# Performance work log

Hardware: AMD Instinct MI355X
Metric: run time of the kernel (lower is better)

Reference implementation:

```python
import jax, jax.numpy as jnp
import numpy as np
import math

N = 100000
E = 800000
H = 256
TDIM = 32
NTYPES = 22
NLAYERS = 2


def layer_norm(x, g, b, eps=1e-5):
    mu = jnp.mean(x, axis=-1, keepdims=True)
    var = jnp.var(x, axis=-1, keepdims=True)
    return (x - mu) * jax.lax.rsqrt(var + eps) * g + b


def setup_inputs() -> dict:
    key = jax.random.key(0)
    ks = jax.random.split(key, 16)
    s = 1.0 / math.sqrt(H)
    inp = {
        "clause_reprs": jax.random.normal(ks[0], (N, H), dtype=jnp.float32),
        "timestamps": jax.random.uniform(ks[1], (N,), dtype=jnp.float32) * 10000.0,
        "deriv_types": jax.random.randint(ks[2], (N,), 0, NTYPES),
        "derivation_edges": jax.random.randint(ks[3], (2, E), 0, N),
        # params
        "emb_table": jax.random.normal(ks[4], (NTYPES, H), dtype=jnp.float32),
        "temp_W": jax.random.normal(ks[5], (TDIM, H), dtype=jnp.float32) / math.sqrt(TDIM),
        "temp_b": jnp.zeros((H,), jnp.float32),
        "fus_W1": jax.random.normal(ks[6], (3 * H, H), dtype=jnp.float32) / math.sqrt(3 * H),
        "fus_b1": jnp.zeros((H,), jnp.float32),
        "fus_W2": jax.random.normal(ks[7], (H, H), dtype=jnp.float32) * s,
        "fus_b2": jnp.zeros((H,), jnp.float32),
        "in_g": jnp.ones((H,), jnp.float32),
        "in_b": jnp.zeros((H,), jnp.float32),
        "deriv_W": jax.random.normal(ks[8], (NLAYERS, 2 * H, H), dtype=jnp.float32) / math.sqrt(2 * H),
        "deriv_b": jnp.zeros((NLAYERS, H), jnp.float32),
        "dn_g": jnp.ones((NLAYERS, H), jnp.float32),
        "dn_b": jnp.zeros((NLAYERS, H), jnp.float32),
    }
    return inp


def reference(clause_reprs, timestamps, deriv_types, derivation_edges,
              emb_table, temp_W, temp_b, fus_W1, fus_b1, fus_W2, fus_b2,
              in_g, in_b, deriv_W, deriv_b, dn_g, dn_b):
    # --- temporal sinusoidal encoding -> projection ---
    half = TDIM // 2
    freqs = jnp.exp(-math.log(10000.0) * jnp.arange(half, dtype=jnp.float32) / half)
    angles = timestamps[:, None] * freqs[None, :]                      # (N, half)
    pe = jnp.concatenate([jnp.sin(angles), jnp.cos(angles)], axis=-1)  # (N, TDIM)
    temporal_enc = pe @ temp_W + temp_b                                # (N, H)
    # --- derivation type embedding ---
    deriv_enc = emb_table[deriv_types]                                 # (N, H)
    # --- input fusion + residual + LN ---
    cat = jnp.concatenate([clause_reprs, temporal_enc, deriv_enc], axis=-1)
    fused = jax.nn.relu(cat @ fus_W1 + fus_b1) @ fus_W2 + fus_b2
    x = layer_norm(fused + clause_reprs, in_g, in_b)
    # --- derivation message passing along DAG edges (parent -> child) ---
    src, dst = derivation_edges[0], derivation_edges[1]
    count = jnp.zeros((N, 1), jnp.float32).at[dst].add(1.0)
    count = jnp.maximum(count, 1.0)
    for l in range(NLAYERS):
        parent_msgs = x[src]                                           # (E, H) gather
        agg = jnp.zeros_like(x).at[dst].add(parent_msgs) / count       # (N, H) scatter-add
        combined = jnp.concatenate([x, agg], axis=-1)                  # (N, 2H)
        update = jax.nn.relu(combined @ deriv_W[l] + deriv_b[l])
        x = layer_norm(x + update, dn_g[l], dn_b[l])
    return x
```

## Files before the change

### kernel.cpp

```cpp
#include <hip/hip_runtime.h>
#include <hip/hip_bf16.h>
#include <math.h>

#define N_NODES 100000
#define N_EDGES 800000
#define H 256
#define NTYPES 22
#define SCAN_G 98
#define GRID5 ((N_NODES + 127) / 128)

typedef __attribute__((ext_vector_type(8))) short short8;
typedef __attribute__((ext_vector_type(4))) float f32x4;
typedef unsigned short u16;

__device__ __forceinline__ u16 f2bf(float f) {
    unsigned u = __float_as_uint(f);
    u += 0x7FFF + ((u >> 16) & 1);
    return (u16)(u >> 16);
}
__device__ __forceinline__ float bf2f(u16 u) {
    return __uint_as_float(((unsigned)u) << 16);
}
__device__ __forceinline__ int pi2(int k) {
    return (k & 192) | ((k & 3) << 4) | ((k >> 2) & 15);
}

__device__ __forceinline__ void gload16(const void* g, void* l) {
    __builtin_amdgcn_global_load_lds(
        (const __attribute__((address_space(1))) unsigned int*)g,
        (__attribute__((address_space(3))) unsigned int*)l, 16, 0, 0);
}

__global__ __launch_bounds__(256) void conv_bf16(
    const float* __restrict__ src, u16* __restrict__ dst)
{
    size_t i = (size_t)blockIdx.x * 256 + threadIdx.x;
    const float4 a = ((const float4*)src)[i * 2];
    const float4 b = ((const float4*)src)[i * 2 + 1];
    short8 v;
    v[0] = (short)f2bf(a.x); v[1] = (short)f2bf(a.y);
    v[2] = (short)f2bf(a.z); v[3] = (short)f2bf(a.w);
    v[4] = (short)f2bf(b.x); v[5] = (short)f2bf(b.y);
    v[6] = (short)f2bf(b.z); v[7] = (short)f2bf(b.w);
    ((short8*)dst)[i] = v;
}

__global__ __launch_bounds__(256) void prep_small(
    const float* __restrict__ temp_W, const float* __restrict__ temp_b,
    const float* __restrict__ emb, const float* __restrict__ fus_W1,
    const float* __restrict__ fus_b1,
    float* __restrict__ C1, float* __restrict__ C2, float* __restrict__ beff)
{
    int b = blockIdx.x;
    int j = threadIdx.x;
    if (b < 32) {
        float acc = 0.f;
        #pragma unroll 8
        for (int m = 0; m < H; ++m)
            acc += temp_W[b * H + m] * fus_W1[(size_t)(H + m) * H + j];
        C1[b * H + j] = acc;
    } else if (b < 32 + NTYPES) {
        int e = b - 32;
        float acc = 0.f;
        #pragma unroll 8
        for (int m = 0; m < H; ++m)
            acc += emb[e * H + m] * fus_W1[(size_t)(2 * H + m) * H + j];
        C2[e * H + j] = acc;
    } else {
        float acc = fus_b1[j];
        #pragma unroll 8
        for (int m = 0; m < H; ++m)
            acc += temp_b[m] * fus_W1[(size_t)(H + m) * H + j];
        beff[j] = acc;
    }
}

__global__ __launch_bounds__(256) void prep_frag(
    const float* __restrict__ fus_W1, const float* __restrict__ C1,
    const float* __restrict__ fus_W2, const float* __restrict__ deriv_W,
    u16* __restrict__ wblob)
{
    int s = blockIdx.x;
    #pragma unroll
    for (int it = 0; it < 4; ++it) {
        int c = it * 256 + threadIdx.x;
        int l = c & 63, nt = c >> 6;
        int ncol = (nt << 4) | (l & 15);
        int kin = (l >> 4) << 3;
        short8 v;
        #pragma unroll
        for (int i = 0; i < 8; ++i) {
            const float* srcp;
            if (s < 8) {
                srcp = fus_W1 + (size_t)(s * 32 + kin + i) * H;
            } else if (s == 8) {
                srcp = C1 + (size_t)(kin + i) * H;
            } else if (s < 17) {
                int k = (s - 9) * 32 + kin + i;
                srcp = fus_W2 + (size_t)pi2(k) * H;
            } else if (s < 33) {
                int k = (s - 17) * 32 + kin + i;
                srcp = deriv_W + (size_t)((k >> 8) * 256 + pi2(k & 255)) * H;
            } else {
                int k = (s - 33) * 32 + kin + i;
                srcp = deriv_W + (size_t)(512 + (k >> 8) * 256 + pi2(k & 255)) * H;
            }
            v[i] = (short)f2bf(srcp[ncol]);
        }
        *reinterpret_cast<short8*>(wblob + (size_t)s * 8192 + (size_t)c * 8) = v;
    }
}

__global__ void count_kernel(const int* __restrict__ dst, int* __restrict__ cnt)
{
    int e = blockIdx.x * blockDim.x + threadIdx.x;
    if (e < N_EDGES) atomicAdd(&cnt[dst[e]], 1);
}

__global__ __launch_bounds__(1024) void scan1_kernel(
    const int* __restrict__ cnt, int* __restrict__ off, int* __restrict__ bsum)
{
    __shared__ int s[1024];
    int i = blockIdx.x * 1024 + threadIdx.x;
    int v = (i < N_NODES) ? cnt[i] : 0;
    s[threadIdx.x] = v;
    __syncthreads();
    #pragma unroll
    for (int o = 1; o < 1024; o <<= 1) {
        int t = (threadIdx.x >= o) ? s[threadIdx.x - o] : 0;
        __syncthreads();
        s[threadIdx.x] += t;
        __syncthreads();
    }
    if (i < N_NODES) off[i] = s[threadIdx.x];
    if (threadIdx.x == 1023) bsum[blockIdx.x] = s[1023];
}

__global__ void scan2_kernel(const int* __restrict__ bsum, int* __restrict__ bbase)
{
    if (threadIdx.x == 0) {
        int acc = 0;
        for (int b = 0; b < SCAN_G; ++b) { bbase[b] = acc; acc += bsum[b]; }
    }
}

__global__ __launch_bounds__(1024) void scan3_kernel(
    int* __restrict__ off, const int* __restrict__ bbase,
    const int* __restrict__ cnt, int* __restrict__ cursor)
{
    int i = blockIdx.x * 1024 + threadIdx.x;
    if (i < N_NODES) {
        int incl = off[i] + bbase[blockIdx.x];
        off[i] = incl;
        cursor[i] = incl - cnt[i];
    }
}

__global__ void fill_kernel(const int* __restrict__ src, const int* __restrict__ dst,
                            int* __restrict__ cursor, int* __restrict__ csr)
{
    int e = blockIdx.x * blockDim.x + threadIdx.x;
    if (e < N_EDGES) {
        int pos = atomicAdd(&cursor[dst[e]], 1);
        csr[pos] = src[e];
    }
}

__global__ __launch_bounds__(256) void gather_kernel(
    const u16* __restrict__ xb, const int* __restrict__ csr,
    const int* __restrict__ off, const int* __restrict__ cnt,
    u16* __restrict__ agg)
{
    int node = blockIdx.x * 4 + (threadIdx.x >> 6);
    int l = threadIdx.x & 63;
    int half = l >> 5, lc = l & 31;
    int deg = cnt[node];
    int start = off[node] - deg;
    float a[8] = {0.f, 0.f, 0.f, 0.f, 0.f, 0.f, 0.f, 0.f};
    int j = half;
    for (; j + 2 < deg; j += 4) {
        int s0 = csr[start + j];
        int s1 = csr[start + j + 2];
        short8 v0 = *reinterpret_cast<const short8*>(xb + (size_t)s0 * H + lc * 8);
        short8 v1 = *reinterpret_cast<const short8*>(xb + (size_t)s1 * H + lc * 8);
        #pragma unroll
        for (int i = 0; i < 8; ++i)
            a[i] += bf2f((u16)v0[i]) + bf2f((u16)v1[i]);
    }
    if (j < deg) {
        int s0 = csr[start + j];
        short8 v0 = *reinterpret_cast<const short8*>(xb + (size_t)s0 * H + lc * 8);
        #pragma unroll
        for (int i = 0; i < 8; ++i)
            a[i] += bf2f((u16)v0[i]);
    }
    #pragma unroll
    for (int i = 0; i < 8; ++i)
        a[i] += __shfl_xor(a[i], 32);
    if (half == 0) {
        float sc = 1.0f / fmaxf((float)deg, 1.0f);
        short8 o;
        #pragma unroll
        for (int i = 0; i < 8; ++i) o[i] = (short)f2bf(a[i] * sc);
        *reinterpret_cast<short8*>(agg + (size_t)node * H + lc * 8) = o;
    }
}

__device__ __forceinline__ void mfma_regs(const short8 a[4], const short8 b[4],
                                          f32x4 acc[4][4])
{
    #pragma unroll
    for (int n = 0; n < 4; ++n)
        #pragma unroll
        for (int m = 0; m < 4; ++m)
            acc[m][n] = __builtin_amdgcn_mfma_f32_16x16x32_bf16(a[m], b[n],
                                                                acc[m][n], 0, 0, 0);
}

__global__ __launch_bounds__(512, 4) void k1_mfma(
    const u16* __restrict__ cb, const float* __restrict__ ts,
    const int* __restrict__ types, const u16* __restrict__ wblob,
    const float* __restrict__ C2, const float* __restrict__ beff,
    u16* __restrict__ hb)
{
    __shared__ __align__(16) u16 Asm[32768];
    __shared__ __align__(16) u16 pes[4096];
    int tid = threadIdx.x, w = tid >> 6, l = tid & 63;
    int wm = w >> 2, wn = w & 3, g = l >> 4, c0 = l & 15;
    int i0 = blockIdx.x * 128;

    #pragma unroll
    for (int j = 0; j < 8; ++j) {
        int rt = j * 16 + (tid >> 5);
        int grow = min(i0 + rt, N_NODES - 1);
        int gl = (l & 31) ^ (rt & 7);
        gload16(cb + (size_t)grow * H + gl * 8,
                Asm + (size_t)rt * 256 + (l & 31) * 8);
    }
    {
        int prow = tid >> 2, kq = tid & 3;
        float tsv = ts[min(i0 + prow, N_NODES - 1)];
        short8 v;
        #pragma unroll
        for (int i = 0; i < 8; ++i) {
            int k = kq * 8 + i;
            float fr = expf(-0.57564627324851f * (float)(k & 15));
            float ang = tsv * fr;
            v[i] = (short)f2bf((k < 16) ? sinf(ang) : cosf(ang));
        }
        *reinterpret_cast<short8*>(pes + prow * 32 + ((kq ^ (prow & 3)) << 3)) = v;
    }
    __syncthreads();

    f32x4 acc[4][4] = {};
    #pragma unroll
    for (int t = 0; t < 9; ++t) {
        short8 a[4], b[4];
        #pragma unroll
        for (int m = 0; m < 4; ++m) {
            int row = (((wm << 2) | m) << 4) + c0;
            if (t < 8) {
                int c = t * 4 + g;
                a[m] = *reinterpret_cast<const short8*>(
                    Asm + row * 256 + ((c ^ (c0 & 7)) << 3));
            } else {
                a[m] = *reinterpret_cast<const short8*>(
                    pes + row * 32 + ((g ^ (c0 & 3)) << 3));
            }
        }
        #pragma unroll
        for (int n = 0; n < 4; ++n)
            b[n] = *reinterpret_cast<const short8*>(
                wblob + (size_t)t * 8192 + (size_t)(((((wn << 2) | n) << 6) | l) << 3));
        mfma_regs(a, b, acc);
    }

    float bev[4];
    #pragma unroll
    for (int n = 0; n < 4; ++n) bev[n] = beff[(((wn << 2) | n) << 4) | c0];
    #pragma unroll
    for (int m = 0; m < 4; ++m) {
        #pragma unroll
        for (int r = 0; r < 4; ++r) {
            int rl = (((wm << 2) | m) << 4) + (g << 2) + r;
            int row = i0 + rl;
            bool ok = row < N_NODES;
            int tp = types[ok ? row : 0];
            const float* c2r = C2 + (size_t)tp * H;
            ushort4 o;
            float v0 = fmaxf(acc[m][0][r] + bev[0] + c2r[((wn << 2) << 4) | c0], 0.f);
            float v1 = fmaxf(acc[m][1][r] + bev[1] + c2r[(((wn << 2) | 1) << 4) | c0], 0.f);
            float v2 = fmaxf(acc[m][2][r] + bev[2] + c2r[(((wn << 2) | 2) << 4) | c0], 0.f);
            float v3 = fmaxf(acc[m][3][r] + bev[3] + c2r[(((wn << 2) | 3) << 4) | c0], 0.f);
            o.x = f2bf(v0); o.y = f2bf(v1); o.z = f2bf(v2); o.w = f2bf(v3);
            if (ok)
                *reinterpret_cast<ushort4*>(hb + (size_t)row * H + (wn << 6) + (c0 << 2)) = o;
        }
    }
}

__global__ __launch_bounds__(512, 4) void k2_mfma(
    const u16* __restrict__ hb, const u16* __restrict__ cb,
    const u16* __restrict__ wblob, const float* __restrict__ b2,
    const float* __restrict__ gW, const float* __restrict__ bW,
    u16* __restrict__ xb)
{
    __shared__ __align__(16) u16 Asm[32768];
    __shared__ float2 red[512];
    int tid = threadIdx.x, w = tid >> 6, l = tid & 63;
    int wm = w >> 2, wn = w & 3, g = l >> 4, c0 = l & 15;
    int i0 = blockIdx.x * 128;

    #pragma unroll
    for (int j = 0; j < 8; ++j) {
        int rt = j * 16 + (tid >> 5);
        int grow = min(i0 + rt, N_NODES - 1);
        int gl = (l & 31) ^ (rt & 7);
        gload16(hb + (size_t)grow * H + gl * 8,
                Asm + (size_t)rt * 256 + (l & 31) * 8);
    }
    __syncthreads();

    f32x4 acc[4][4] = {};
    #pragma unroll
    for (int t = 0; t < 8; ++t) {
        short8 a[4], b[4];
        #pragma unroll
        for (int m = 0; m < 4; ++m) {
            int row = (((wm << 2) | m) << 4) + c0;
            int c = t * 4 + g;
            a[m] = *reinterpret_cast<const short8*>(
                Asm + row * 256 + ((c ^ (c0 & 7)) << 3));
        }
        #pragma unroll
        for (int n = 0; n < 4; ++n)
            b[n] = *reinterpret_cast<const short8*>(
                wblob + (size_t)t * 8192 + (size_t)(((((wn << 2) | n) << 6) | l) << 3));
        mfma_regs(a, b, acc);
    }

    float bv[4], gv[4], bbv[4];
    int lc[4];
    #pragma unroll
    for (int n = 0; n < 4; ++n) {
        lc[n] = (((wn << 2) | n) << 4) | c0;
        bv[n] = b2[lc[n]]; gv[n] = gW[lc[n]]; bbv[n] = bW[lc[n]];
    }
    #pragma unroll
    for (int m = 0; m < 4; ++m) {
        #pragma unroll
        for (int r = 0; r < 4; ++r) {
            int rl = (((wm << 2) | m) << 4) + (g << 2) + r;
            int rowc = min(i0 + rl, N_NODES - 1);
            const u16* cr = cb + (size_t)rowc * H;
            float s = 0.f, q = 0.f;
            #pragma unroll
            for (int n = 0; n < 4; ++n) {
                float pv = acc[m][n][r] + bv[n] + bf2f(cr[lc[n]]);
                acc[m][n][r] = pv;
                s += pv; q += pv * pv;
            }
            #pragma unroll
            for (int o = 1; o < 16; o <<= 1) {
                s += __shfl_xor(s, o);
                q += __shfl_xor(q, o);
            }
            if (c0 == 0) red[(rl << 2) | wn] = make_float2(s, q);
        }
    }
    __syncthreads();
    #pragma unroll
    for (int m = 0; m < 4; ++m) {
        #pragma unroll
        for (int r = 0; r < 4; ++r) {
            int rl = (((wm << 2) | m) << 4) + (g << 2) + r;
            int row = i0 + rl;
            float2 t0 = red[(rl << 2) | 0], t1 = red[(rl << 2) | 1];
            float2 t2 = red[(rl << 2) | 2], t3 = red[(rl << 2) | 3];
            float S = t0.x + t1.x + t2.x + t3.x;
            float Q = t0.y + t1.y + t2.y + t3.y;
            float mu = S * (1.0f / 256.0f);
            float rstd = rsqrtf(Q * (1.0f / 256.0f) - mu * mu + 1e-5f);
            if (row < N_NODES) {
                ushort4 o;
                o.x = f2bf((acc[m][0][r] - mu) * rstd * gv[0] + bbv[0]);
                o.y = f2bf((acc[m][1][r] - mu) * rstd * gv[1] + bbv[1]);
                o.z = f2bf((acc[m][2][r] - mu) * rstd * gv[2] + bbv[2]);
                o.w = f2bf((acc[m][3][r] - mu) * rstd * gv[3] + bbv[3]);
                *reinterpret_cast<ushort4*>(xb + (size_t)row * H + (wn << 6) + (c0 << 2)) = o;
            }
        }
    }
}

template<bool FINAL>
__global__ __launch_bounds__(512, 2) void k5_mfma(
    const u16* __restrict__ xb, const u16* __restrict__ aggb,
    const u16* __restrict__ wblob, const float* __restrict__ bl,
    const float* __restrict__ gl_, const float* __restrict__ bnl,
    u16* __restrict__ xbout, float* __restrict__ xout)
{
    __shared__ __align__(16) u16 Asm[65536];
    __shared__ float2 red[512];
    int tid = threadIdx.x, w = tid >> 6, l = tid & 63;
    int wm = w >> 2, wn = w & 3, g = l >> 4, c0 = l & 15;
    int i0 = blockIdx.x * 128;

    #pragma unroll
    for (int j = 0; j < 16; ++j) {
        int rt = j * 8 + w;
        int grow = min(i0 + rt, N_NODES - 1);
        int gl = l ^ w;
        const u16* src = (gl < 32)
            ? xb + (size_t)grow * H + gl * 8
            : aggb + (size_t)grow * H + (gl - 32) * 8;
        gload16(src, Asm + (size_t)rt * 512 + l * 8);
    }
    __syncthreads();

    f32x4 acc[4][4] = {};
    #pragma unroll
    for (int t = 0; t < 16; ++t) {
        short8 a[4], b[4];
        #pragma unroll
        for (int m = 0; m < 4; ++m) {
            int row = (((wm << 2) | m) << 4) + c0;
            int c = t * 4 + g;
            a[m] = *reinterpret_cast<const short8*>(
                Asm + row * 512 + ((c ^ (c0 & 7)) << 3));
        }
        #pragma unroll
        for (int n = 0; n < 4; ++n)
            b[n] = *reinterpret_cast<const short8*>(
                wblob + (size_t)t * 8192 + (size_t)(((((wn << 2) | n) << 6) | l) << 3));
        mfma_regs(a, b, acc);
    }

    float bv[4], gv[4], bbv[4];
    int lc[4];
    #pragma unroll
    for (int n = 0; n < 4; ++n) {
        lc[n] = (((wn << 2) | n) << 4) | c0;
        bv[n] = bl[lc[n]]; gv[n] = gl_[lc[n]]; bbv[n] = bnl[lc[n]];
    }
    int g0 = (wn << 3) + (c0 >> 1);
    #pragma unroll
    for (int m = 0; m < 4; ++m) {
        #pragma unroll
        for (int r = 0; r < 4; ++r) {
            int rl = (((wm << 2) | m) << 4) + (g << 2) + r;
            ushort4 xr = *reinterpret_cast<const ushort4*>(
                Asm + rl * 512 + ((g0 ^ (rl & 7)) << 3) + ((c0 & 1) << 2));
            float p0 = bf2f(xr.x) + fmaxf(acc[m][0][r] + bv[0], 0.f);
            float p1 = bf2f(xr.y) + fmaxf(acc[m][1][r] + bv[1], 0.f);
            float p2 = bf2f(xr.z) + fmaxf(acc[m][2][r] + bv[2], 0.f);
            float p3 = bf2f(xr.w) + fmaxf(acc[m][3][r] + bv[3], 0.f);
            acc[m][0][r] = p0; acc[m][1][r] = p1;
            acc[m][2][r] = p2; acc[m][3][r] = p3;
            float s = p0 + p1 + p2 + p3;
            float q = p0 * p0 + p1 * p1 + p2 * p2 + p3 * p3;
            #pragma unroll
            for (int o = 1; o < 16; o <<= 1) {
                s += __shfl_xor(s, o);
                q += __shfl_xor(q, o);
            }
            if (c0 == 0) red[(rl << 2) | wn] = make_float2(s, q);
        }
    }
    __syncthreads();
    #pragma unroll
    for (int m = 0; m < 4; ++m) {
        #pragma unroll
        for (int r = 0; r < 4; ++r) {
            int rl = (((wm << 2) | m) << 4) + (g << 2) + r;
            int row = i0 + rl;
            float2 t0 = red[(rl << 2) | 0], t1 = red[(rl << 2) | 1];
            float2 t2 = red[(rl << 2) | 2], t3 = red[(rl << 2) | 3];
            float S = t0.x + t1.x + t2.x + t3.x;
            float Q = t0.y + t1.y + t2.y + t3.y;
            float mu = S * (1.0f / 256.0f);
            float rstd = rsqrtf(Q * (1.0f / 256.0f) - mu * mu + 1e-5f);
            if (row < N_NODES) {
                if (FINAL) {
                    #pragma unroll
                    for (int n = 0; n < 4; ++n)
                        xout[(size_t)row * H + lc[n]] =
                            (acc[m][n][r] - mu) * rstd * gv[n] + bbv[n];
                } else {
                    ushort4 o;
                    o.x = f2bf((acc[m][0][r] - mu) * rstd * gv[0] + bbv[0]);
                    o.y = f2bf((acc[m][1][r] - mu) * rstd * gv[1] + bbv[1]);
                    o.z = f2bf((acc[m][2][r] - mu) * rstd * gv[2] + bbv[2]);
                    o.w = f2bf((acc[m][3][r] - mu) * rstd * gv[3] + bbv[3]);
                    *reinterpret_cast<ushort4*>(
                        xbout + (size_t)row * H + (wn << 6) + (c0 << 2)) = o;
                }
            }
        }
    }
}

extern "C" void kernel_launch(void* const* d_in, const int* in_sizes, int n_in,
                              void* d_out, int out_size, void* d_ws, size_t ws_size,
                              hipStream_t stream)
{
    const float* clause  = (const float*)d_in[0];
    const float* ts      = (const float*)d_in[1];
    const int*   types   = (const int*)  d_in[2];
    const int*   edges   = (const int*)  d_in[3];
    const float* emb     = (const float*)d_in[4];
    const float* temp_W  = (const float*)d_in[5];
    const float* temp_b  = (const float*)d_in[6];
    const float* fus_W1  = (const float*)d_in[7];
    const float* fus_b1  = (const float*)d_in[8];
    const float* fus_W2  = (const float*)d_in[9];
    const float* fus_b2  = (const float*)d_in[10];
    const float* in_g    = (const float*)d_in[11];
    const float* in_b    = (const float*)d_in[12];
    const float* deriv_W = (const float*)d_in[13];
    const float* deriv_b = (const float*)d_in[14];
    const float* dn_g    = (const float*)d_in[15];
    const float* dn_b    = (const float*)d_in[16];

    char* p = (char*)d_ws;
    float* C1   = (float*)p;            p += 32 * H * 4;
    float* C2   = (float*)p;            p += NTYPES * H * 4;
    float* beff = (float*)p;            p += H * 4;
    int* cnt    = (int*)p;              p += N_NODES * 4;
    int* off    = (int*)p;              p += N_NODES * 4;
    int* cursor = (int*)p;              p += N_NODES * 4;
    int* bsum   = (int*)p;              p += 128 * 4;
    int* bbase  = (int*)p;              p += 128 * 4;
    int* csr    = (int*)p;              p += N_EDGES * 4;
    u16* wblob  = (u16*)p;              p += 49 * 8192 * 2;
    u16* B1     = (u16*)p;              p += (size_t)N_NODES * H * 2;
    u16* B2     = (u16*)p;              p += (size_t)N_NODES * H * 2;
    float* x    = (float*)d_out;

    const int* src = edges;
    const int* dst = edges + N_EDGES;

    conv_bf16<<<(N_NODES * H / 8 + 255) / 256, 256, 0, stream>>>(clause, B1);
    prep_small<<<32 + NTYPES + 1, 256, 0, stream>>>(temp_W, temp_b, emb, fus_W1,
                                                    fus_b1, C1, C2, beff);
    prep_frag<<<49, 256, 0, stream>>>(fus_W1, C1, fus_W2, deriv_W, wblob);

    hipMemsetAsync(cnt, 0, N_NODES * sizeof(int), stream);
    count_kernel<<<(N_EDGES + 255) / 256, 256, 0, stream>>>(dst, cnt);
    scan1_kernel<<<SCAN_G, 1024, 0, stream>>>(cnt, off, bsum);
    scan2_kernel<<<1, 64, 0, stream>>>(bsum, bbase);
    scan3_kernel<<<SCAN_G, 1024, 0, stream>>>(off, bbase, cnt, cursor);
    fill_kernel<<<(N_EDGES + 255) / 256, 256, 0, stream>>>(src, dst, cursor, csr);

    k1_mfma<<<GRID5, 512, 0, stream>>>(B1, ts, types, wblob, C2, beff, B2);
    k2_mfma<<<GRID5, 512, 0, stream>>>(B2, B1, wblob + (size_t)9 * 8192,
                                       fus_b2, in_g, in_b, B2);

    gather_kernel<<<N_NODES / 4, 256, 0, stream>>>(B2, csr, off, cnt, B1);
    k5_mfma<false><<<GRID5, 512, 0, stream>>>(
        B2, B1, wblob + (size_t)17 * 8192, deriv_b, dn_g, dn_b, B2, nullptr);
    gather_kernel<<<N_NODES / 4, 256, 0, stream>>>(B2, csr, off, cnt, B1);
    k5_mfma<true><<<GRID5, 512, 0, stream>>>(
        B2, B1, wblob + (size_t)33 * 8192, deriv_b + H, dn_g + H, dn_b + H,
        nullptr, x);
}
```

Before: 580.8 us.

## Load GEMM A operands directly from global memory instead of staging through LDS

The three MFMA GEMM kernels stop copying their 128-row A tiles into shared memory with global_load_lds and a barrier. Each lane now reads its short8 A fragments straight from global memory, relying on L1/L2 for reuse across the four column-group waves. In k1, each lane computes its sinusoidal PE fragment in registers instead of through an LDS buffer. Dropping the 64 KB LDS buffer lets k5 raise its launch bound from 2 to 4 blocks, at the cost of more uncoalesced global loads and redundant traffic.

```diff
diff --git a/kernel.cpp b/kernel.cpp
--- a/kernel.cpp
+++ b/kernel.cpp
@@ -23,12 +23,6 @@
 }
 __device__ __forceinline__ int pi2(int k) {
     return (k & 192) | ((k & 3) << 4) | ((k >> 2) & 15);
-}
-
-__device__ __forceinline__ void gload16(const void* g, void* l) {
-    __builtin_amdgcn_global_load_lds(
-        (const __attribute__((address_space(1))) unsigned int*)g,
-        (__attribute__((address_space(3))) unsigned int*)l, 16, 0, 0);
 }
 
 __global__ __launch_bounds__(256) void conv_bf16(
@@ -223,55 +217,50 @@
     const float* __restrict__ C2, const float* __restrict__ beff,
     u16* __restrict__ hb)
 {
-    __shared__ __align__(16) u16 Asm[32768];
-    __shared__ __align__(16) u16 pes[4096];
     int tid = threadIdx.x, w = tid >> 6, l = tid & 63;
     int wm = w >> 2, wn = w & 3, g = l >> 4, c0 = l & 15;
     int i0 = blockIdx.x * 128;
 
-    #pragma unroll
-    for (int j = 0; j < 8; ++j) {
-        int rt = j * 16 + (tid >> 5);
-        int grow = min(i0 + rt, N_NODES - 1);
-        int gl = (l & 31) ^ (rt & 7);
-        gload16(cb + (size_t)grow * H + gl * 8,
-                Asm + (size_t)rt * 256 + (l & 31) * 8);
+    int rows[4];
+    size_t rowo[4];
+    #pragma unroll
+    for (int m = 0; m < 4; ++m) {
+        rows[m] = min(i0 + ((((wm << 2) | m) << 4) | c0), N_NODES - 1);
+        rowo[m] = (size_t)rows[m] * H;
+    }
+    const u16* wb = wblob + ((((wn << 2) << 6) | l) << 3);
+    int kg = g << 3;
+
+    f32x4 acc[4][4] = {};
+    #pragma unroll
+    for (int t = 0; t < 8; ++t) {
+        short8 a[4], b[4];
+        #pragma unroll
+        for (int m = 0; m < 4; ++m)
+            a[m] = *reinterpret_cast<const short8*>(cb + rowo[m] + t * 32 + kg);
+        #pragma unroll
+        for (int n = 0; n < 4; ++n)
+            b[n] = *reinterpret_cast<const short8*>(wb + (size_t)t * 8192 + n * 512);
+        mfma_regs(a, b, acc);
     }
     {
-        int prow = tid >> 2, kq = tid & 3;
-        float tsv = ts[min(i0 + prow, N_NODES - 1)];
-        short8 v;
-        #pragma unroll
-        for (int i = 0; i < 8; ++i) {
-            int k = kq * 8 + i;
-            float fr = expf(-0.57564627324851f * (float)(k & 15));
-            float ang = tsv * fr;
-            v[i] = (short)f2bf((k < 16) ? sinf(ang) : cosf(ang));
-        }
-        *reinterpret_cast<short8*>(pes + prow * 32 + ((kq ^ (prow & 3)) << 3)) = v;
-    }
-    __syncthreads();
-
-    f32x4 acc[4][4] = {};
-    #pragma unroll
-    for (int t = 0; t < 9; ++t) {
         short8 a[4], b[4];
         #pragma unroll
         for (int m = 0; m < 4; ++m) {
-            int row = (((wm << 2) | m) << 4) + c0;
-            if (t < 8) {
-                int c = t * 4 + g;
-                a[m] = *reinterpret_cast<const short8*>(
-                    Asm + row * 256 + ((c ^ (c0 & 7)) << 3));
-            } else {
-                a[m] = *reinterpret_cast<const short8*>(
-                    pes + row * 32 + ((g ^ (c0 & 3)) << 3));
-            }
+            float tsv = ts[rows[m]];
+            short8 v;
+            #pragma unroll
+            for (int i = 0; i < 8; ++i) {
+                int k = kg + i;
+                float fr = expf(-0.57564627324851f * (float)(k & 15));
+                float ang = tsv * fr;
+                v[i] = (short)f2bf((k < 16) ? sinf(ang) : cosf(ang));
+            }
+            a[m] = v;
         }
         #pragma unroll
         for (int n = 0; n < 4; ++n)
-            b[n] = *reinterpret_cast<const short8*>(
-                wblob + (size_t)t * 8192 + (size_t)(((((wn << 2) | n) << 6) | l) << 3));
+            b[n] = *reinterpret_cast<const short8*>(wb + (size_t)8 * 8192 + n * 512);
         mfma_regs(a, b, acc);
     }
 
@@ -305,37 +294,28 @@
     const float* __restrict__ gW, const float* __restrict__ bW,
     u16* __restrict__ xb)
 {
-    __shared__ __align__(16) u16 Asm[32768];
     __shared__ float2 red[512];
     int tid = threadIdx.x, w = tid >> 6, l = tid & 63;
     int wm = w >> 2, wn = w & 3, g = l >> 4, c0 = l & 15;
     int i0 = blockIdx.x * 128;
 
-    #pragma unroll
-    for (int j = 0; j < 8; ++j) {
-        int rt = j * 16 + (tid >> 5);
-        int grow = min(i0 + rt, N_NODES - 1);
-        int gl = (l & 31) ^ (rt & 7);
-        gload16(hb + (size_t)grow * H + gl * 8,
-                Asm + (size_t)rt * 256 + (l & 31) * 8);
-    }
-    __syncthreads();
+    size_t rowo[4];
+    #pragma unroll
+    for (int m = 0; m < 4; ++m)
+        rowo[m] = (size_t)min(i0 + ((((wm << 2) | m) << 4) | c0), N_NODES - 1) * H;
+    const u16* wb = wblob + ((((wn << 2) << 6) | l) << 3);
+    int kg = g << 3;
 
     f32x4 acc[4][4] = {};
     #pragma unroll
     for (int t = 0; t < 8; ++t) {
         short8 a[4], b[4];
         #pragma unroll
-        for (int m = 0; m < 4; ++m) {
-            int row = (((wm << 2) | m) << 4) + c0;
-            int c = t * 4 + g;
-            a[m] = *reinterpret_cast<const short8*>(
-                Asm + row * 256 + ((c ^ (c0 & 7)) << 3));
-        }
+        for (int m = 0; m < 4; ++m)
+            a[m] = *reinterpret_cast<const short8*>(hb + rowo[m] + t * 32 + kg);
         #pragma unroll
         for (int n = 0; n < 4; ++n)
-            b[n] = *reinterpret_cast<const short8*>(
-                wblob + (size_t)t * 8192 + (size_t)(((((wn << 2) | n) << 6) | l) << 3));
+            b[n] = *reinterpret_cast<const short8*>(wb + (size_t)t * 8192 + n * 512);
         mfma_regs(a, b, acc);
     }
 
@@ -394,45 +374,36 @@
 }
 
 template<bool FINAL>
-__global__ __launch_bounds__(512, 2) void k5_mfma(
+__global__ __launch_bounds__(512, 4) void k5_mfma(
     const u16* __restrict__ xb, const u16* __restrict__ aggb,
     const u16* __restrict__ wblob, const float* __restrict__ bl,
     const float* __restrict__ gl_, const float* __restrict__ bnl,
     u16* __restrict__ xbout, float* __restrict__ xout)
 {
-    __shared__ __align__(16) u16 Asm[65536];
     __shared__ float2 red[512];
     int tid = threadIdx.x, w = tid >> 6, l = tid & 63;
     int wm = w >> 2, wn = w & 3, g = l >> 4, c0 = l & 15;
     int i0 = blockIdx.x * 128;
 
-    #pragma unroll
-    for (int j = 0; j < 16; ++j) {
-        int rt = j * 8 + w;
-        int grow = min(i0 + rt, N_NODES - 1);
-        int gl = l ^ w;
-        const u16* src = (gl < 32)
-            ? xb + (size_t)grow * H + gl * 8
-            : aggb + (size_t)grow * H + (gl - 32) * 8;
-        gload16(src, Asm + (size_t)rt * 512 + l * 8);
-    }
-    __syncthreads();
+    size_t rowo[4];
+    #pragma unroll
+    for (int m = 0; m < 4; ++m)
+        rowo[m] = (size_t)min(i0 + ((((wm << 2) | m) << 4) | c0), N_NODES - 1) * H;
+    const u16* wb = wblob + ((((wn << 2) << 6) | l) << 3);
+    int kg = g << 3;
 
     f32x4 acc[4][4] = {};
     #pragma unroll
     for (int t = 0; t < 16; ++t) {
+        const u16* Ab = (t < 8) ? xb : aggb;
+        int ko = (t & 7) * 32 + kg;
         short8 a[4], b[4];
         #pragma unroll
-        for (int m = 0; m < 4; ++m) {
-            int row = (((wm << 2) | m) << 4) + c0;
-            int c = t * 4 + g;
-            a[m] = *reinterpret_cast<const short8*>(
-                Asm + row * 512 + ((c ^ (c0 & 7)) << 3));
-        }
+        for (int m = 0; m < 4; ++m)
+            a[m] = *reinterpret_cast<const short8*>(Ab + rowo[m] + ko);
         #pragma unroll
         for (int n = 0; n < 4; ++n)
-            b[n] = *reinterpret_cast<const short8*>(
-                wblob + (size_t)t * 8192 + (size_t)(((((wn << 2) | n) << 6) | l) << 3));
+            b[n] = *reinterpret_cast<const short8*>(wb + (size_t)t * 8192 + n * 512);
         mfma_regs(a, b, acc);
     }
 
@@ -443,14 +414,14 @@
         lc[n] = (((wn << 2) | n) << 4) | c0;
         bv[n] = bl[lc[n]]; gv[n] = gl_[lc[n]]; bbv[n] = bnl[lc[n]];
     }
-    int g0 = (wn << 3) + (c0 >> 1);
     #pragma unroll
     for (int m = 0; m < 4; ++m) {
         #pragma unroll
         for (int r = 0; r < 4; ++r) {
             int rl = (((wm << 2) | m) << 4) + (g << 2) + r;
+            int rowc = min(i0 + rl, N_NODES - 1);
             ushort4 xr = *reinterpret_cast<const ushort4*>(
-                Asm + rl * 512 + ((g0 ^ (rl & 7)) << 3) + ((c0 & 1) << 2));
+                xb + (size_t)rowc * H + (wn << 6) + (c0 << 2));
             float p0 = bf2f(xr.x) + fmaxf(acc[m][0][r] + bv[0], 0.f);
             float p1 = bf2f(xr.y) + fmaxf(acc[m][1][r] + bv[1], 0.f);
             float p2 = bf2f(xr.z) + fmaxf(acc[m][2][r] + bv[2], 0.f);
```

Result: slower. 747.6 us (+28.7%).
